# Performance work log

Hardware: AMD Instinct MI355X
Metric: run time of the kernel (lower is better)

## Reference

```python
import jax, jax.numpy as jnp
import numpy as np

N, D, M, E, K = 16384, 512, 1024, 8, 2
LOSS_COEF = 0.01
EPS = 1e-10


def setup_inputs() -> dict:
    key = jax.random.key(0)
    ks = jax.random.split(key, 6)
    x = jax.random.normal(ks[0], (N, D), dtype=jnp.float32)
    # gate weight (torch init is zeros; use small random so routing is non-degenerate)
    w_gate = 0.02 * jax.random.normal(ks[1], (D, E), dtype=jnp.float32)
    # stacked expert FFN params: Linear(D->M), GELU, Linear(M->D)
    W1 = jax.random.normal(ks[2], (E, D, M), dtype=jnp.float32) / np.sqrt(D)
    b1 = jnp.zeros((E, M), dtype=jnp.float32)
    W2 = jax.random.normal(ks[3], (E, M, D), dtype=jnp.float32) / np.sqrt(M)
    b2 = jnp.zeros((E, D), dtype=jnp.float32)
    return {"x": x, "w_gate": w_gate, "W1": W1, "b1": b1, "W2": W2, "b2": b2}


def _cv_squared(v):
    # torch .var() is unbiased (ddof=1)
    v = v.astype(jnp.float32)
    return jnp.var(v, ddof=1) / (jnp.mean(v) ** 2 + EPS)


def reference(x, w_gate, W1, b1, W2, b2):
    n = x.shape[0]
    # --- noisy_top_k_gating (eval path: no noise) ---
    logits = x @ w_gate                                  # [N, E]
    top_logits, top_idx = jax.lax.top_k(logits, min(K + 1, E))
    topk_logits = top_logits[:, :K]                      # [N, K]
    topk_idx = top_idx[:, :K]                            # [N, K]
    topk_gates = jax.nn.softmax(topk_logits, axis=-1)    # [N, K]
    gates = jnp.zeros_like(logits).at[jnp.arange(n)[:, None], topk_idx].set(topk_gates)
    importance = gates.sum(axis=0)                       # [E]
    load = (gates > 0).sum(axis=0).astype(jnp.float32)   # [E]
    loss = LOSS_COEF * (_cv_squared(importance) + _cv_squared(load))
    # --- experts (dense equivalent of sparse dispatch/combine: gate==0 rows contribute 0) ---
    h = jnp.einsum('nd,edm->enm', x, W1) + b1[:, None, :]     # [E, N, M]
    h = jax.nn.gelu(h, approximate=False)
    out = jnp.einsum('enm,emd->end', h, W2) + b2[:, None, :]  # [E, N, D]
    y = jnp.einsum('ne,end->nd', gates, out)                  # [N, D]
    return (y, loss)
```

## Files before the change

### kernel.cpp

```cpp
#include <hip/hip_runtime.h>
#include <math.h>

#define NTOK 16384
#define DDIM 512
#define MDIM 1024
#define NEXP 8
#define TMAX 264

typedef __attribute__((ext_vector_type(8))) short short8;
typedef __attribute__((ext_vector_type(4))) float floatx4;

__device__ inline unsigned short f2bf(float f){
  union { float f; unsigned int u; } v; v.f = f;
  unsigned int u = v.u;
  u += ((u >> 16) & 1u) + 0x7fffu;
  return (unsigned short)(u >> 16);
}

__device__ inline float bf2f(unsigned short s){
  union { unsigned int u; float f; } v;
  v.u = ((unsigned int)s) << 16;
  return v.f;
}

__device__ inline float gelu_fast(float x){
  float u = x * 0.70710678118654752f;
  float a = fabsf(u);
  float t = __builtin_amdgcn_rcpf(fmaf(0.3275911f, a, 1.0f));
  float p = fmaf(1.061405429f, t, -1.453152027f);
  p = fmaf(p, t, 1.421413741f);
  p = fmaf(p, t, -0.284496736f);
  p = fmaf(p, t, 0.254829592f);
  p = p * t;
  float e = __expf(-u * u);
  float erfa = fmaf(-p, e, 1.0f);
  float erfu = copysignf(erfa, u);
  return 0.5f * x * (1.0f + erfu);
}

__device__ __forceinline__ void gload16(const unsigned short* g, unsigned short* l){
  __builtin_amdgcn_global_load_lds(
      (const __attribute__((address_space(1))) void*)g,
      (__attribute__((address_space(3))) void*)l,
      16, 0, 0);
}


__global__ void init_small_kernel(int* counts, float* imp){
  int t = threadIdx.x;
  if (t < NEXP){ counts[t] = 0; imp[t] = 0.0f; }
}

__global__ void transpose_conv_kernel(const float* __restrict__ in,
                                      unsigned short* __restrict__ out,
                                      int R, int C){
  __shared__ float tile[32][33];
  int e  = blockIdx.z;
  int c0 = blockIdx.x << 5;
  int r0 = blockIdx.y << 5;
  const float* src = in + (size_t)e * R * C;
  unsigned short* dst = out + (size_t)e * R * C;
  int tc = threadIdx.x;
  int tr = threadIdx.y;
  #pragma unroll
  for (int i = 0; i < 32; i += 8)
    tile[tr + i][tc] = src[(size_t)(r0 + tr + i) * C + c0 + tc];
  __syncthreads();
  #pragma unroll
  for (int i = 0; i < 32; i += 8)
    dst[(size_t)(c0 + tr + i) * R + r0 + tc] = f2bf(tile[tc][tr + i]);
}


__global__ __launch_bounds__(256)
void gating_kernel(const float* __restrict__ x,
                   const float* __restrict__ wg,
                   unsigned short* __restrict__ xb,
                   int* __restrict__ tok_e, float* __restrict__ tok_g,
                   int* __restrict__ counts, float* __restrict__ imp){
  __shared__ int   lcnt[NEXP];
  __shared__ float limp[NEXP];
  int t = threadIdx.x;
  if (t < NEXP){ lcnt[t] = 0; limp[t] = 0.0f; }
  __syncthreads();

  int wave = t >> 6;
  int lane = t & 63;

  for (int it = 0; it < 16; it++){
    int n = blockIdx.x * 64 + it * 4 + wave;

    const float4* xp = (const float4*)(x + (size_t)n * DDIM + lane * 8);
    float4 a = xp[0], b = xp[1];
    float xv[8] = {a.x, a.y, a.z, a.w, b.x, b.y, b.z, b.w};

    short8 xo;
    #pragma unroll
    for (int j = 0; j < 8; j++) xo[j] = (short)f2bf(xv[j]);
    *(short8*)(xb + (size_t)n * DDIM + lane * 8) = xo;

    double acc[NEXP];
    #pragma unroll
    for (int e = 0; e < NEXP; e++) acc[e] = 0.0;
    #pragma unroll
    for (int j = 0; j < 8; j++){
      const float* wr = wg + (size_t)(lane * 8 + j) * NEXP;
      #pragma unroll
      for (int e = 0; e < NEXP; e++) acc[e] += (double)xv[j] * (double)wr[e];
    }
    #pragma unroll
    for (int off = 32; off >= 1; off >>= 1){
      #pragma unroll
      for (int e = 0; e < NEXP; e++) acc[e] += __shfl_xor(acc[e], off);
    }
    if (lane == 0){
      int i0 = -1, i1 = -1;
      double l0 = -1e300, l1 = -1e300;
      #pragma unroll
      for (int e = 0; e < NEXP; e++){
        double v = acc[e];
        if (v > l0){ l1 = l0; i1 = i0; l0 = v; i0 = e; }
        else if (v > l1){ l1 = v; i1 = e; }
      }
      float ex = expf((float)(l1 - l0));
      float g0 = 1.0f / (1.0f + ex);
      float g1 = ex / (1.0f + ex);
      tok_e[n * 2]     = i0; tok_e[n * 2 + 1] = i1;
      tok_g[n * 2]     = g0; tok_g[n * 2 + 1] = g1;
      atomicAdd(&lcnt[i0], 1); atomicAdd(&lcnt[i1], 1);
      atomicAdd(&limp[i0], g0); atomicAdd(&limp[i1], g1);
    }
  }
  __syncthreads();
  if (t < NEXP){
    atomicAdd(&counts[t], lcnt[t]);
    atomicAdd(&imp[t], limp[t]);
  }
}

__global__ void loss_scan_kernel(const int* __restrict__ counts,
                                 const float* __restrict__ imp,
                                 int* __restrict__ offsets, int* __restrict__ cursor,
                                 int* __restrict__ tile_pre,
                                 float* __restrict__ out_loss){
  int off = 0, tp = 0;
  double si = 0, si2 = 0, sl = 0, sl2 = 0;
  for (int e = 0; e < NEXP; e++){
    offsets[e] = off; cursor[e] = off;
    tile_pre[e] = tp;
    tp += (counts[e] + 127) >> 7;
    off += counts[e];
    double im = (double)imp[e];
    double ld = (double)counts[e];
    si += im; si2 += im * im;
    sl += ld; sl2 += ld * ld;
  }
  offsets[NEXP] = off;
  tile_pre[NEXP] = tp;
  double mi = si / 8.0, ml = sl / 8.0;
  double vi = (si2 - 8.0 * mi * mi) / 7.0;
  double vl = (sl2 - 8.0 * ml * ml) / 7.0;
  double loss = 0.01 * (vi / (mi * mi + 1e-10) + vl / (ml * ml + 1e-10));
  *out_loss = (float)loss;
}

__global__ __launch_bounds__(256)
void scatter_kernel(const int* __restrict__ tok_e,
                    int* __restrict__ cursor,
                    int* __restrict__ btok, int* __restrict__ slot_of){
  __shared__ int lcnt[NEXP];
  __shared__ int lbase[NEXP];
  int t = threadIdx.x;
  if (t < NEXP) lcnt[t] = 0;
  __syncthreads();

  int n = blockIdx.x * 256 + t;
  int e0 = tok_e[n * 2], e1 = tok_e[n * 2 + 1];
  int r0 = atomicAdd(&lcnt[e0], 1);
  int r1 = atomicAdd(&lcnt[e1], 1);
  __syncthreads();
  if (t < NEXP) lbase[t] = atomicAdd(&cursor[t], lcnt[t]);
  __syncthreads();
  int s0 = lbase[e0] + r0;
  int s1 = lbase[e1] + r1;
  btok[s0] = n;
  btok[s1] = n;
  slot_of[n * 2]     = s0;
  slot_of[n * 2 + 1] = s1;
}


__global__ __launch_bounds__(256)
void gemm1_kernel(const unsigned short* __restrict__ xb,
                  const unsigned short* __restrict__ w1t,
                  const float* __restrict__ b1,
                  const int* __restrict__ offsets,
                  const int* __restrict__ tile_pre,
                  const int* __restrict__ btok,
                  unsigned short* __restrict__ H){
  int ct = blockIdx.x / TMAX;
  int tt = blockIdx.x % TMAX;
  if (tt >= tile_pre[NEXP]) return;
  int e = 0;
  while (tt >= tile_pre[e + 1]) e++;
  int rt = tt - tile_pre[e];
  int off = offsets[e];
  int cnt = offsets[e + 1] - off;
  int r0 = rt << 7;

  __shared__ unsigned short AsLo[128 * 32];
  __shared__ unsigned short AsHi[128 * 32];
  __shared__ unsigned short BsLo[128 * 32];
  __shared__ unsigned short BsHi[128 * 32];

  int t = threadIdx.x;
  int srow = t >> 2;
  int scol = (t & 3) << 3;
  int w = t >> 6;

  int ra0 = r0 + srow;        if (ra0 >= cnt) ra0 = cnt - 1;
  int ra1 = r0 + 64 + srow;   if (ra1 >= cnt) ra1 = cnt - 1;
  const unsigned short* aptr0 = xb + (size_t)btok[off + ra0] * DDIM + scol;
  const unsigned short* aptr1 = xb + (size_t)btok[off + ra1] * DDIM + scol;
  const unsigned short* bptr0 = w1t + ((size_t)e * MDIM + (ct << 7) + srow) * DDIM + scol;
  const unsigned short* bptr1 = bptr0 + (size_t)64 * DDIM;

  int lane = t & 63;
  int wr = (w >> 1) << 6;
  int wc = (w & 1) << 6;
  int lm = lane & 15;
  int lq = lane >> 4;

  floatx4 acc[4][4] = {};
  for (int k0 = 0; k0 < DDIM; k0 += 64){
    gload16(aptr0 + k0,      AsLo + w * 512);
    gload16(aptr0 + k0 + 32, AsHi + w * 512);
    gload16(aptr1 + k0,      AsLo + 2048 + w * 512);
    gload16(aptr1 + k0 + 32, AsHi + 2048 + w * 512);
    gload16(bptr0 + k0,      BsLo + w * 512);
    gload16(bptr0 + k0 + 32, BsHi + w * 512);
    gload16(bptr1 + k0,      BsLo + 2048 + w * 512);
    gload16(bptr1 + k0 + 32, BsHi + 2048 + w * 512);
    __syncthreads();
    #pragma unroll
    for (int h = 0; h < 2; h++){
      const unsigned short* Ap = h ? AsHi : AsLo;
      const unsigned short* Bp = h ? BsHi : BsLo;
      short8 af[4], bf[4];
      #pragma unroll
      for (int i = 0; i < 4; i++) af[i] = *(const short8*)&Ap[(wr + i * 16 + lm) * 32 + lq * 8];
      #pragma unroll
      for (int j = 0; j < 4; j++) bf[j] = *(const short8*)&Bp[(wc + j * 16 + lm) * 32 + lq * 8];
      #pragma unroll
      for (int i = 0; i < 4; i++)
        #pragma unroll
        for (int j = 0; j < 4; j++)
          acc[i][j] = __builtin_amdgcn_mfma_f32_16x16x32_bf16(bf[j], af[i], acc[i][j], 0, 0, 0);
    }
    __syncthreads();
  }

  const float* bias = b1 + e * MDIM + (ct << 7) + wc;
  #pragma unroll
  for (int i = 0; i < 4; i++){
    int tokl = r0 + wr + i * 16 + lm;
    bool valid = tokl < cnt;
    unsigned short* hrow = H + (size_t)(off + (valid ? tokl : 0)) * MDIM + (ct << 7) + wc;
    #pragma unroll
    for (int j = 0; j < 4; j++){
      float4 bv = *(const float4*)(bias + j * 16 + lq * 4);
      float g0 = gelu_fast(acc[i][j][0] + bv.x);
      float g1 = gelu_fast(acc[i][j][1] + bv.y);
      float g2 = gelu_fast(acc[i][j][2] + bv.z);
      float g3 = gelu_fast(acc[i][j][3] + bv.w);
      uint2 p;
      p.x = (unsigned)f2bf(g0) | ((unsigned)f2bf(g1) << 16);
      p.y = (unsigned)f2bf(g2) | ((unsigned)f2bf(g3) << 16);
      if (valid) *(uint2*)(hrow + j * 16 + lq * 4) = p;
    }
  }
}

__global__ __launch_bounds__(256)
void gemm2_kernel(const unsigned short* __restrict__ H,
                  const unsigned short* __restrict__ w2t,
                  const float* __restrict__ b2,
                  const int* __restrict__ offsets,
                  const int* __restrict__ tile_pre,
                  unsigned short* __restrict__ O){
  int ct = blockIdx.x / TMAX;
  int tt = blockIdx.x % TMAX;
  if (tt >= tile_pre[NEXP]) return;
  int e = 0;
  while (tt >= tile_pre[e + 1]) e++;
  int rt = tt - tile_pre[e];
  int off = offsets[e];
  int cnt = offsets[e + 1] - off;
  int r0 = rt << 7;

  __shared__ unsigned short AsLo[128 * 32];
  __shared__ unsigned short AsHi[128 * 32];
  __shared__ unsigned short BsLo[128 * 32];
  __shared__ unsigned short BsHi[128 * 32];

  int t = threadIdx.x;
  int srow = t >> 2;
  int scol = (t & 3) << 3;
  int w = t >> 6;

  int ra0 = r0 + srow;        if (ra0 >= cnt) ra0 = cnt - 1;
  int ra1 = r0 + 64 + srow;   if (ra1 >= cnt) ra1 = cnt - 1;
  const unsigned short* aptr0 = H + (size_t)(off + ra0) * MDIM + scol;
  const unsigned short* aptr1 = H + (size_t)(off + ra1) * MDIM + scol;
  const unsigned short* bptr0 = w2t + ((size_t)e * DDIM + (ct << 7) + srow) * MDIM + scol;
  const unsigned short* bptr1 = bptr0 + (size_t)64 * MDIM;

  int lane = t & 63;
  int wr = (w >> 1) << 6;
  int wc = (w & 1) << 6;
  int lm = lane & 15;
  int lq = lane >> 4;

  floatx4 acc[4][4] = {};
  for (int k0 = 0; k0 < MDIM; k0 += 64){
    gload16(aptr0 + k0,      AsLo + w * 512);
    gload16(aptr0 + k0 + 32, AsHi + w * 512);
    gload16(aptr1 + k0,      AsLo + 2048 + w * 512);
    gload16(aptr1 + k0 + 32, AsHi + 2048 + w * 512);
    gload16(bptr0 + k0,      BsLo + w * 512);
    gload16(bptr0 + k0 + 32, BsHi + w * 512);
    gload16(bptr1 + k0,      BsLo + 2048 + w * 512);
    gload16(bptr1 + k0 + 32, BsHi + 2048 + w * 512);
    __syncthreads();
    #pragma unroll
    for (int h = 0; h < 2; h++){
      const unsigned short* Ap = h ? AsHi : AsLo;
      const unsigned short* Bp = h ? BsHi : BsLo;
      short8 af[4], bf[4];
      #pragma unroll
      for (int i = 0; i < 4; i++) af[i] = *(const short8*)&Ap[(wr + i * 16 + lm) * 32 + lq * 8];
      #pragma unroll
      for (int j = 0; j < 4; j++) bf[j] = *(const short8*)&Bp[(wc + j * 16 + lm) * 32 + lq * 8];
      #pragma unroll
      for (int i = 0; i < 4; i++)
        #pragma unroll
        for (int j = 0; j < 4; j++)
          acc[i][j] = __builtin_amdgcn_mfma_f32_16x16x32_bf16(bf[j], af[i], acc[i][j], 0, 0, 0);
    }
    __syncthreads();
  }

  const float* bias = b2 + e * DDIM + (ct << 7) + wc;
  #pragma unroll
  for (int i = 0; i < 4; i++){
    int tokl = r0 + wr + i * 16 + lm;
    bool valid = tokl < cnt;
    unsigned short* orow = O + (size_t)(off + (valid ? tokl : 0)) * DDIM + (ct << 7) + wc;
    #pragma unroll
    for (int j = 0; j < 4; j++){
      float4 bv = *(const float4*)(bias + j * 16 + lq * 4);
      uint2 p;
      p.x = (unsigned)f2bf(acc[i][j][0] + bv.x) | ((unsigned)f2bf(acc[i][j][1] + bv.y) << 16);
      p.y = (unsigned)f2bf(acc[i][j][2] + bv.z) | ((unsigned)f2bf(acc[i][j][3] + bv.w) << 16);
      if (valid) *(uint2*)(orow + j * 16 + lq * 4) = p;
    }
  }
}


__global__ __launch_bounds__(256)
void combine_kernel(const unsigned short* __restrict__ O,
                    const float* __restrict__ tok_g,
                    const int* __restrict__ slot_of,
                    float* __restrict__ y){
  int wave = threadIdx.x >> 6;
  int lane = threadIdx.x & 63;
  int n = blockIdx.x * 4 + wave;
  int s0 = slot_of[n * 2], s1 = slot_of[n * 2 + 1];
  float g0 = tok_g[n * 2], g1 = tok_g[n * 2 + 1];
  short8 a = *(const short8*)(O + (size_t)s0 * DDIM + lane * 8);
  short8 b = *(const short8*)(O + (size_t)s1 * DDIM + lane * 8);
  float4 o0, o1;
  float* po0 = (float*)&o0;
  float* po1 = (float*)&o1;
  #pragma unroll
  for (int j = 0; j < 4; j++){
    po0[j] = g0 * bf2f((unsigned short)a[j]) + g1 * bf2f((unsigned short)b[j]);
    po1[j] = g0 * bf2f((unsigned short)a[j + 4]) + g1 * bf2f((unsigned short)b[j + 4]);
  }
  float4* yp = (float4*)(y + (size_t)n * DDIM + lane * 8);
  yp[0] = o0;
  yp[1] = o1;
}


extern "C" void kernel_launch(void* const* d_in, const int* in_sizes, int n_in,
                              void* d_out, int out_size, void* d_ws, size_t ws_size,
                              hipStream_t stream){
  const float* x  = (const float*)d_in[0];
  const float* wg = (const float*)d_in[1];
  const float* W1 = (const float*)d_in[2];
  const float* b1 = (const float*)d_in[3];
  const float* W2 = (const float*)d_in[4];
  const float* b2 = (const float*)d_in[5];
  float* y = (float*)d_out;

  char* ws = (char*)d_ws;
  size_t o = 0;
  auto alloc = [&](size_t bytes)->char*{
    char* p = ws + o;
    o += (bytes + 255) & ~(size_t)255;
    return p;
  };
  unsigned short* xb   = (unsigned short*)alloc((size_t)NTOK * DDIM * 2);
  unsigned short* w1t  = (unsigned short*)alloc((size_t)NEXP * MDIM * DDIM * 2);
  unsigned short* w2t  = (unsigned short*)alloc((size_t)NEXP * DDIM * MDIM * 2);
  unsigned short* H    = (unsigned short*)alloc((size_t)NTOK * 2 * MDIM * 2);
  unsigned short* O    = (unsigned short*)alloc((size_t)NTOK * 2 * DDIM * 2);
  int*   btok    = (int*)  alloc((size_t)NTOK * 2 * 4);
  int*   slot_of = (int*)  alloc((size_t)NTOK * 2 * 4);
  int*   tok_e   = (int*)  alloc((size_t)NTOK * 2 * 4);
  float* tok_g   = (float*)alloc((size_t)NTOK * 2 * 4);
  int*   counts  = (int*)  alloc(64);
  float* imp     = (float*)alloc(64);
  int*   offsets = (int*)  alloc(64);
  int*   cursor  = (int*)  alloc(64);
  int*   tile_pre= (int*)  alloc(64);

  hipLaunchKernelGGL(init_small_kernel, dim3(1), dim3(64), 0, stream, counts, imp);
  hipLaunchKernelGGL(transpose_conv_kernel, dim3(MDIM / 32, DDIM / 32, NEXP), dim3(32, 8), 0, stream,
                     W1, w1t, DDIM, MDIM);
  hipLaunchKernelGGL(transpose_conv_kernel, dim3(DDIM / 32, MDIM / 32, NEXP), dim3(32, 8), 0, stream,
                     W2, w2t, MDIM, DDIM);
  hipLaunchKernelGGL(gating_kernel, dim3(NTOK / 64), dim3(256), 0, stream,
                     x, wg, xb, tok_e, tok_g, counts, imp);
  hipLaunchKernelGGL(loss_scan_kernel, dim3(1), dim3(1), 0, stream,
                     counts, imp, offsets, cursor, tile_pre, y + (size_t)NTOK * DDIM);
  hipLaunchKernelGGL(scatter_kernel, dim3(NTOK / 256), dim3(256), 0, stream,
                     tok_e, cursor, btok, slot_of);
  hipLaunchKernelGGL(gemm1_kernel, dim3(TMAX * 8), dim3(256), 0, stream,
                     xb, w1t, b1, offsets, tile_pre, btok, H);
  hipLaunchKernelGGL(gemm2_kernel, dim3(TMAX * 4), dim3(256), 0, stream,
                     H, w2t, b2, offsets, tile_pre, O);
  hipLaunchKernelGGL(combine_kernel, dim3(NTOK / 4), dim3(256), 0, stream,
                     O, tok_g, slot_of, y);
}
```

Baseline: 309.5 us.

## Double-buffer LDS tiles in expert GEMMs to overlap loads with MFMA

Both expert GEMM kernels now use ping-pong shared-memory buffers with a K step of 32. The next slice's global-to-LDS load is issued before computing on the current slice, and one barrier per iteration replaces the previous two. The aim is to hide global load latency behind MFMA work. The cost is twice as many iterations with smaller work per barrier, and correctness depends on gload16's wait semantics across the single barrier.

```diff
diff --git a/kernel.cpp b/kernel.cpp
--- a/kernel.cpp
+++ b/kernel.cpp
@@ -208,10 +208,8 @@
   int cnt = offsets[e + 1] - off;
   int r0 = rt << 7;
 
-  __shared__ unsigned short AsLo[128 * 32];
-  __shared__ unsigned short AsHi[128 * 32];
-  __shared__ unsigned short BsLo[128 * 32];
-  __shared__ unsigned short BsHi[128 * 32];
+  __shared__ unsigned short As[2][128 * 32];
+  __shared__ unsigned short Bs[2][128 * 32];
 
   int t = threadIdx.x;
   int srow = t >> 2;
@@ -231,33 +229,34 @@
   int lm = lane & 15;
   int lq = lane >> 4;
 
+  gload16(aptr0, &As[0][w * 512]);
+  gload16(aptr1, &As[0][2048 + w * 512]);
+  gload16(bptr0, &Bs[0][w * 512]);
+  gload16(bptr1, &Bs[0][2048 + w * 512]);
+
   floatx4 acc[4][4] = {};
-  for (int k0 = 0; k0 < DDIM; k0 += 64){
-    gload16(aptr0 + k0,      AsLo + w * 512);
-    gload16(aptr0 + k0 + 32, AsHi + w * 512);
-    gload16(aptr1 + k0,      AsLo + 2048 + w * 512);
-    gload16(aptr1 + k0 + 32, AsHi + 2048 + w * 512);
-    gload16(bptr0 + k0,      BsLo + w * 512);
-    gload16(bptr0 + k0 + 32, BsHi + w * 512);
-    gload16(bptr1 + k0,      BsLo + 2048 + w * 512);
-    gload16(bptr1 + k0 + 32, BsHi + 2048 + w * 512);
+  int p = 0;
+  #pragma unroll 4
+  for (int ki = 0; ki < DDIM / 32; ki++){
     __syncthreads();
-    #pragma unroll
-    for (int h = 0; h < 2; h++){
-      const unsigned short* Ap = h ? AsHi : AsLo;
-      const unsigned short* Bp = h ? BsHi : BsLo;
-      short8 af[4], bf[4];
+    if (ki + 1 < DDIM / 32){
+      int k0 = (ki + 1) * 32;
+      gload16(aptr0 + k0, &As[p ^ 1][w * 512]);
+      gload16(aptr1 + k0, &As[p ^ 1][2048 + w * 512]);
+      gload16(bptr0 + k0, &Bs[p ^ 1][w * 512]);
+      gload16(bptr1 + k0, &Bs[p ^ 1][2048 + w * 512]);
+    }
+    short8 af[4], bf[4];
+    #pragma unroll
+    for (int i = 0; i < 4; i++) af[i] = *(const short8*)&As[p][(wr + i * 16 + lm) * 32 + lq * 8];
+    #pragma unroll
+    for (int j = 0; j < 4; j++) bf[j] = *(const short8*)&Bs[p][(wc + j * 16 + lm) * 32 + lq * 8];
+    #pragma unroll
+    for (int i = 0; i < 4; i++)
       #pragma unroll
-      for (int i = 0; i < 4; i++) af[i] = *(const short8*)&Ap[(wr + i * 16 + lm) * 32 + lq * 8];
-      #pragma unroll
-      for (int j = 0; j < 4; j++) bf[j] = *(const short8*)&Bp[(wc + j * 16 + lm) * 32 + lq * 8];
-      #pragma unroll
-      for (int i = 0; i < 4; i++)
-        #pragma unroll
-        for (int j = 0; j < 4; j++)
-          acc[i][j] = __builtin_amdgcn_mfma_f32_16x16x32_bf16(bf[j], af[i], acc[i][j], 0, 0, 0);
-    }
-    __syncthreads();
+      for (int j = 0; j < 4; j++)
+        acc[i][j] = __builtin_amdgcn_mfma_f32_16x16x32_bf16(bf[j], af[i], acc[i][j], 0, 0, 0);
+    p ^= 1;
   }
 
   const float* bias = b1 + e * MDIM + (ct << 7) + wc;
@@ -273,10 +272,10 @@
       float g1 = gelu_fast(acc[i][j][1] + bv.y);
       float g2 = gelu_fast(acc[i][j][2] + bv.z);
       float g3 = gelu_fast(acc[i][j][3] + bv.w);
-      uint2 p;
-      p.x = (unsigned)f2bf(g0) | ((unsigned)f2bf(g1) << 16);
-      p.y = (unsigned)f2bf(g2) | ((unsigned)f2bf(g3) << 16);
-      if (valid) *(uint2*)(hrow + j * 16 + lq * 4) = p;
+      uint2 pk;
+      pk.x = (unsigned)f2bf(g0) | ((unsigned)f2bf(g1) << 16);
+      pk.y = (unsigned)f2bf(g2) | ((unsigned)f2bf(g3) << 16);
+      if (valid) *(uint2*)(hrow + j * 16 + lq * 4) = pk;
     }
   }
 }
@@ -298,10 +297,8 @@
   int cnt = offsets[e + 1] - off;
   int r0 = rt << 7;
 
-  __shared__ unsigned short AsLo[128 * 32];
-  __shared__ unsigned short AsHi[128 * 32];
-  __shared__ unsigned short BsLo[128 * 32];
-  __shared__ unsigned short BsHi[128 * 32];
+  __shared__ unsigned short As[2][128 * 32];
+  __shared__ unsigned short Bs[2][128 * 32];
 
   int t = threadIdx.x;
   int srow = t >> 2;
@@ -321,33 +318,34 @@
   int lm = lane & 15;
   int lq = lane >> 4;
 
+  gload16(aptr0, &As[0][w * 512]);
+  gload16(aptr1, &As[0][2048 + w * 512]);
+  gload16(bptr0, &Bs[0][w * 512]);
+  gload16(bptr1, &Bs[0][2048 + w * 512]);
+
   floatx4 acc[4][4] = {};
-  for (int k0 = 0; k0 < MDIM; k0 += 64){
-    gload16(aptr0 + k0,      AsLo + w * 512);
-    gload16(aptr0 + k0 + 32, AsHi + w * 512);
-    gload16(aptr1 + k0,      AsLo + 2048 + w * 512);
-    gload16(aptr1 + k0 + 32, AsHi + 2048 + w * 512);
-    gload16(bptr0 + k0,      BsLo + w * 512);
-    gload16(bptr0 + k0 + 32, BsHi + w * 512);
-    gload16(bptr1 + k0,      BsLo + 2048 + w * 512);
-    gload16(bptr1 + k0 + 32, BsHi + 2048 + w * 512);
+  int p = 0;
+  #pragma unroll 4
+  for (int ki = 0; ki < MDIM / 32; ki++){
     __syncthreads();
-    #pragma unroll
-    for (int h = 0; h < 2; h++){
-      const unsigned short* Ap = h ? AsHi : AsLo;
-      const unsigned short* Bp = h ? BsHi : BsLo;
-      short8 af[4], bf[4];
+    if (ki + 1 < MDIM / 32){
+      int k0 = (ki + 1) * 32;
+      gload16(aptr0 + k0, &As[p ^ 1][w * 512]);
+      gload16(aptr1 + k0, &As[p ^ 1][2048 + w * 512]);
+      gload16(bptr0 + k0, &Bs[p ^ 1][w * 512]);
+      gload16(bptr1 + k0, &Bs[p ^ 1][2048 + w * 512]);
+    }
+    short8 af[4], bf[4];
+    #pragma unroll
+    for (int i = 0; i < 4; i++) af[i] = *(const short8*)&As[p][(wr + i * 16 + lm) * 32 + lq * 8];
+    #pragma unroll
+    for (int j = 0; j < 4; j++) bf[j] = *(const short8*)&Bs[p][(wc + j * 16 + lm) * 32 + lq * 8];
+    #pragma unroll
+    for (int i = 0; i < 4; i++)
       #pragma unroll
-      for (int i = 0; i < 4; i++) af[i] = *(const short8*)&Ap[(wr + i * 16 + lm) * 32 + lq * 8];
-      #pragma unroll
-      for (int j = 0; j < 4; j++) bf[j] = *(const short8*)&Bp[(wc + j * 16 + lm) * 32 + lq * 8];
-      #pragma unroll
-      for (int i = 0; i < 4; i++)
-        #pragma unroll
-        for (int j = 0; j < 4; j++)
-          acc[i][j] = __builtin_amdgcn_mfma_f32_16x16x32_bf16(bf[j], af[i], acc[i][j], 0, 0, 0);
-    }
-    __syncthreads();
+      for (int j = 0; j < 4; j++)
+        acc[i][j] = __builtin_amdgcn_mfma_f32_16x16x32_bf16(bf[j], af[i], acc[i][j], 0, 0, 0);
+    p ^= 1;
   }
 
   const float* bias = b2 + e * DDIM + (ct << 7) + wc;
@@ -359,10 +357,10 @@
     #pragma unroll
     for (int j = 0; j < 4; j++){
       float4 bv = *(const float4*)(bias + j * 16 + lq * 4);
-      uint2 p;
-      p.x = (unsigned)f2bf(acc[i][j][0] + bv.x) | ((unsigned)f2bf(acc[i][j][1] + bv.y) << 16);
-      p.y = (unsigned)f2bf(acc[i][j][2] + bv.z) | ((unsigned)f2bf(acc[i][j][3] + bv.w) << 16);
-      if (valid) *(uint2*)(orow + j * 16 + lq * 4) = p;
+      uint2 pk;
+      pk.x = (unsigned)f2bf(acc[i][j][0] + bv.x) | ((unsigned)f2bf(acc[i][j][1] + bv.y) << 16);
+      pk.y = (unsigned)f2bf(acc[i][j][2] + bv.z) | ((unsigned)f2bf(acc[i][j][3] + bv.w) << 16);
+      if (valid) *(uint2*)(orow + j * 16 + lq * 4) = pk;
     }
   }
 }
```

Result: slower. 332.8 us (+7.5%).
